# Performance work log

Hardware: AMD Instinct MI355X
Metric: run time of the kernel (lower is better)

Reference implementation:

```python
import jax, jax.numpy as jnp
import numpy as np

DIM = 64   # voxel grid resolution per axis
C = 64     # channels (C_in == num_outputs, required by residual add)
N = 200000 # number of points
EPS = 1e-3 # keras BatchNormalization default epsilon

def _bn(x, g, b, m, v):
    # inference-mode batch norm
    return (x - m) * jax.lax.rsqrt(v + EPS) * g + b

def _conv3d_relu(x, k, b):
    # x: [1,X,Y,Z,Cin], k: [3,3,3,Cin,Cout] (DHWIO), 'same' padding, relu activation
    y = jax.lax.conv_general_dilated(x, k, (1, 1, 1), 'SAME',
        dimension_numbers=('NDHWC', 'DHWIO', 'NDHWC'))
    return jax.nn.relu(y + b)

def _trilinear(grid, pts):
    # grid: [X,Y,Z,C], pts: [N,3] in voxel coordinates
    dmax = jnp.asarray(grid.shape[:3], pts.dtype) - 1.0
    p = jnp.clip(pts, 0.0, dmax)
    f = jnp.floor(p)
    t = p - f  # [N,3] fractional part
    i0 = f.astype(jnp.int32)
    i1 = jnp.minimum(i0 + 1, jnp.asarray(grid.shape[:3], jnp.int32) - 1)
    out = jnp.zeros((pts.shape[0], grid.shape[-1]), grid.dtype)
    for dx in (0, 1):
        for dy in (0, 1):
            for dz in (0, 1):
                ix = i1[:, 0] if dx else i0[:, 0]
                iy = i1[:, 1] if dy else i0[:, 1]
                iz = i1[:, 2] if dz else i0[:, 2]
                w = ((t[:, 0] if dx else 1.0 - t[:, 0])
                     * (t[:, 1] if dy else 1.0 - t[:, 1])
                     * (t[:, 2] if dz else 1.0 - t[:, 2]))
                out = out + w[:, None] * grid[ix, iy, iz]
    return out

def setup_inputs():
    key = jax.random.key(0)
    ks = jax.random.split(key, 10)
    inputs = jax.random.normal(ks[0], (N, C), jnp.float32)
    # pt_coords already scaled into voxel space (VOXEL_SIZE_INV folded in)
    pt_coords = jax.random.uniform(ks[1], (N, 3), jnp.float32) * (DIM - 1)
    voxel_indexes = jax.random.randint(ks[2], (N, 3), 0, DIM)
    pts_per_voxel_inv = jax.random.uniform(ks[3], (1, DIM, DIM, DIM, 1), jnp.float32)
    s = 1.0 / np.sqrt(C)
    w_mlp = jax.random.normal(ks[4], (C, C), jnp.float32) * s
    b_mlp = jnp.zeros((C,), jnp.float32)
    sk = 1.0 / np.sqrt(27 * C)
    k1 = jax.random.normal(ks[5], (3, 3, 3, C, C), jnp.float32) * sk
    cb1 = jnp.zeros((C,), jnp.float32)
    k2 = jax.random.normal(ks[6], (3, 3, 3, C, C), jnp.float32) * sk
    cb2 = jnp.zeros((C,), jnp.float32)
    def bn_params(k):
        a, b_, c = jax.random.split(k, 3)
        g = 1.0 + 0.1 * jax.random.normal(a, (C,), jnp.float32)
        be = 0.1 * jax.random.normal(b_, (C,), jnp.float32)
        m = 0.1 * jax.random.normal(c, (C,), jnp.float32)
        v = jnp.ones((C,), jnp.float32)
        return g, be, m, v
    g0, be0, m0, v0 = bn_params(ks[7])
    g1, be1, m1, v1 = bn_params(ks[8])
    g2, be2, m2, v2 = bn_params(ks[9])
    return dict(inputs=inputs, pt_coords=pt_coords, voxel_indexes=voxel_indexes,
                pts_per_voxel_inv=pts_per_voxel_inv, w_mlp=w_mlp, b_mlp=b_mlp,
                g0=g0, be0=be0, m0=m0, v0=v0, k1=k1, cb1=cb1, g1=g1, be1=be1,
                m1=m1, v1=v1, k2=k2, cb2=cb2, g2=g2, be2=be2, m2=m2, v2=v2)

def reference(inputs, pt_coords, voxel_indexes, pts_per_voxel_inv, w_mlp, b_mlp,
              g0, be0, m0, v0, k1, cb1, g1, be1, m1, v1, k2, cb2, g2, be2, m2, v2):
    # point branch: Dense(relu) + BN
    mlp_out = _bn(jax.nn.relu(inputs @ w_mlp + b_mlp), g0, be0, m0, v0)
    # voxelize: scatter_nd adds duplicate-index contributions
    voxels = jnp.zeros((DIM, DIM, DIM, C), inputs.dtype).at[
        voxel_indexes[:, 0], voxel_indexes[:, 1], voxel_indexes[:, 2]].add(inputs)
    voxels = voxels[None] * pts_per_voxel_inv  # per-voxel mean normalization
    # voxel branch: two Conv3D(relu)+BN
    h = _bn(_conv3d_relu(voxels, k1, cb1), g1, be1, m1, v1)
    h = _bn(_conv3d_relu(h, k2, cb2), g2, be2, m2, v2)
    # devoxelize: trilinear gather back to points (coords already in voxel space)
    vox_out = _trilinear(h[0], pt_coords)
    return mlp_out + vox_out
```

## Files before the change

### kernel.cpp

```cpp
#include <hip/hip_runtime.h>
#include <hip/hip_bf16.h>

#define DIMV 64
#define CH 64
#define EPSB 1e-3f

using bf16x8 = __attribute__((ext_vector_type(8))) short;
using f32x16 = __attribute__((ext_vector_type(16))) float;

__device__ __forceinline__ unsigned short f2bf(float f) {
    union { float f; unsigned u; } x; x.f = f;
    unsigned r = x.u + 0x7fff + ((x.u >> 16) & 1);
    return (unsigned short)(r >> 16);
}
__device__ __forceinline__ float bf2f(unsigned short u) {
    union { unsigned u; float f; } x; x.u = ((unsigned)u) << 16;
    return x.f;
}

__global__ __launch_bounds__(256) void mlp_mfma(
    const float* __restrict__ x, const unsigned short* __restrict__ wfrag,
    const float* __restrict__ b, const float* __restrict__ g,
    const float* __restrict__ be, const float* __restrict__ m,
    const float* __restrict__ v, float* __restrict__ out, int npts) {
    const int wid = blockIdx.x * 4 + (threadIdx.x >> 6);
    if (wid * 32 >= npts) return;
    const int lane = threadIdx.x & 63;
    const int col = lane & 31;
    const int kg = lane >> 5;
    const int p0 = wid * 32;

    bf16x8 a[4];
    const float* xr = x + (size_t)(p0 + col) * CH + kg * 8;
#pragma unroll
    for (int kk = 0; kk < 4; ++kk) {
        const float* p = xr + kk * 16;
        bf16x8 t;
#pragma unroll
        for (int j = 0; j < 8; ++j) t[j] = (short)f2bf(p[j]);
        a[kk] = t;
    }

    f32x16 acc[2];
#pragma unroll
    for (int nt = 0; nt < 2; ++nt)
#pragma unroll
        for (int r = 0; r < 16; ++r) acc[nt][r] = 0.f;

#pragma unroll
    for (int kk = 0; kk < 4; ++kk) {
        bf16x8 b0 = *(const bf16x8*)(wfrag + (kk * 2 + 0) * 512 + lane * 8);
        bf16x8 b1 = *(const bf16x8*)(wfrag + (kk * 2 + 1) * 512 + lane * 8);
        acc[0] = __builtin_amdgcn_mfma_f32_32x32x16_bf16(a[kk], b0, acc[0], 0, 0, 0);
        acc[1] = __builtin_amdgcn_mfma_f32_32x32x16_bf16(a[kk], b1, acc[1], 0, 0, 0);
    }

#pragma unroll
    for (int nt = 0; nt < 2; ++nt) {
        int co = nt * 32 + col;
        float scale = g[co] * rsqrtf(v[co] + EPSB);
        float shift = be[co] - m[co] * scale;
        float bias = b[co];
#pragma unroll
        for (int r = 0; r < 16; ++r) {
            int row = (r & 3) + 8 * (r >> 2) + 4 * kg;
            float val = fmaxf(acc[nt][r] + bias, 0.f) * scale + shift;
            out[(size_t)(p0 + row) * CH + co] = val;
        }
    }
}

__global__ void scatter_kernel(const float* __restrict__ x, const int* __restrict__ idx,
                               float* __restrict__ grid, int n_total) {
    int tid = blockIdx.x * blockDim.x + threadIdx.x;
    if (tid >= n_total) return;
    int n = tid >> 6, c = tid & 63;
    int ix = idx[n * 3 + 0], iy = idx[n * 3 + 1], iz = idx[n * 3 + 2];
    atomicAdd(&grid[(size_t)(((ix * DIMV) + iy) * DIMV + iz) * CH + c], x[tid]);
}

__global__ void pack_kernel(const float* __restrict__ A, const float* __restrict__ inv,
                            unsigned short* __restrict__ G1) {
    int t = blockIdx.x * 256 + threadIdx.x;
    if (t >= (DIMV * DIMV * DIMV * CH) / 8) return;
    int v = t >> 3, c8 = (t & 7) * 8;
    const float* src = A + (size_t)v * CH + c8;
    float s = inv[v];
    __align__(16) unsigned short tmp[8];
#pragma unroll
    for (int j = 0; j < 8; ++j) tmp[j] = f2bf(src[j] * s);
    *(int4*)(G1 + (size_t)t * 8) = *(const int4*)tmp;
}

__global__ void wprep_kernel(const float* __restrict__ K, unsigned short* __restrict__ wbuf) {
    int t = blockIdx.x * 256 + threadIdx.x;
    if (t >= 27 * 4 * 2 * 64 * 8) return;
    int j = t & 7;
    int l = (t >> 3) & 63;
    int nt = (t >> 9) & 1;
    int kkl = (t >> 10) & 3;
    int d = t >> 12;
    int ci = kkl * 16 + (l >> 5) * 8 + j;
    int co = nt * 32 + (l & 31);
    wbuf[t] = f2bf(K[((size_t)d * 64 + ci) * 64 + co]);
}

__global__ void wprep_mlp(const float* __restrict__ W, unsigned short* __restrict__ wm) {
    int t = blockIdx.x * 256 + threadIdx.x;
    if (t >= 4 * 2 * 64 * 8) return;
    int j = t & 7;
    int l = (t >> 3) & 63;
    int nt = (t >> 9) & 1;
    int kkl = (t >> 10) & 3;
    int ci = kkl * 16 + (l >> 5) * 8 + j;
    int co = nt * 32 + (l & 31);
    wm[t] = f2bf(W[(size_t)ci * 64 + co]);
}

template <typename OutT>
__global__ __launch_bounds__(256) void conv_mfma(
    const unsigned short* __restrict__ G, const unsigned short* __restrict__ wbuf,
    const float* __restrict__ cb, const float* __restrict__ g,
    const float* __restrict__ be, const float* __restrict__ m,
    const float* __restrict__ v, OutT* __restrict__ out) {
    __shared__ __align__(16) unsigned short slab[288 * 128];
    const int tid = threadIdx.x;
    const int lane = tid & 63;
    const int w = tid >> 6;
    const int wx = w >> 1, wy = w & 1;
    const int lz = lane & 31;
    const int kg = lane >> 5;
    const int BX = blockIdx.x, BY = blockIdx.y, BZ = blockIdx.z;
    const int x0 = 2 * BX - 1, y0 = 2 * BY - 1;
    const int zbase = 32 * BZ - 2;

#pragma unroll
    for (int it = 0; it < 18; ++it) {
        int idx = it * 256 + tid;
        int s = idx & 15;
        int r = idx >> 4;
        int zp = r % 18;
        int ryx = r / 18;
        int xx = x0 + (ryx >> 2);
        int yy = y0 + (ryx & 3);
        int cp = s ^ (zp & 15);
        int c = cp >> 1, p = cp & 1;
        int zz = zbase + 2 * zp + p;
        int4 val = make_int4(0, 0, 0, 0);
        if ((unsigned)xx < DIMV && (unsigned)yy < DIMV && (unsigned)zz < DIMV)
            val = *(const int4*)(G + (size_t)(((xx * DIMV) + yy) * DIMV + zz) * CH + c * 8);
        *(int4*)(slab + (size_t)idx * 8) = val;
    }
    __syncthreads();

    f32x16 acc[2];
#pragma unroll
    for (int nt = 0; nt < 2; ++nt)
#pragma unroll
        for (int r = 0; r < 16; ++r) acc[nt][r] = 0.f;

    bf16x8 bfr0[8], bfr1[8];
#pragma unroll
    for (int q = 0; q < 8; ++q)
        bfr0[q] = *(const bf16x8*)(wbuf + q * 512 + lane * 8);

#pragma unroll
    for (int d = 0; d < 27; ++d) {
        if (d < 26) {
            const unsigned short* wn = wbuf + (size_t)(d + 1) * 4096;
            if (d & 1) {
#pragma unroll
                for (int q = 0; q < 8; ++q) bfr0[q] = *(const bf16x8*)(wn + q * 512 + lane * 8);
            } else {
#pragma unroll
                for (int q = 0; q < 8; ++q) bfr1[q] = *(const bf16x8*)(wn + q * 512 + lane * 8);
            }
        }
        const int dx = d / 9, dy = (d / 3) % 3, dz = d % 3;
        const int zval = lz + dz + 1;
        const int zp = zval >> 1, p = zval & 1;
        const int r0 = ((wx + dx) * 4 + (wy + dy)) * 18 + zp;
#pragma unroll
        for (int kkl = 0; kkl < 4; ++kkl) {
            const int c = kkl * 2 + kg;
            const int slot = (c * 2 + p) ^ (zp & 15);
            bf16x8 a = *(const bf16x8*)(slab + r0 * 128 + slot * 8);
            bf16x8 b0 = (d & 1) ? bfr1[kkl * 2 + 0] : bfr0[kkl * 2 + 0];
            bf16x8 b1 = (d & 1) ? bfr1[kkl * 2 + 1] : bfr0[kkl * 2 + 1];
            acc[0] = __builtin_amdgcn_mfma_f32_32x32x16_bf16(a, b0, acc[0], 0, 0, 0);
            acc[1] = __builtin_amdgcn_mfma_f32_32x32x16_bf16(a, b1, acc[1], 0, 0, 0);
        }
    }

    const int x_out = 2 * BX + wx;
    const int y_out = 2 * BY + wy;
#pragma unroll
    for (int nt = 0; nt < 2; ++nt) {
        int co = nt * 32 + lz;
        float scale = g[co] * rsqrtf(v[co] + EPSB);
        float shift = be[co] - m[co] * scale;
        float bias = cb[co];
        size_t base = (size_t)((x_out * DIMV) + y_out) * DIMV * CH + co;
#pragma unroll
        for (int r = 0; r < 16; ++r) {
            int zrow = (r & 3) + 8 * (r >> 2) + 4 * kg;
            int z = BZ * 32 + zrow;
            float val = fmaxf(acc[nt][r] + bias, 0.f) * scale + shift;
            out[base + (size_t)z * CH] = f2bf(val);
        }
    }
}

__global__ void gather_kernel(const unsigned short* __restrict__ grid,
                              const float* __restrict__ pts,
                              float* __restrict__ out, int n_total) {
    int tid = blockIdx.x * blockDim.x + threadIdx.x;
    if (tid >= n_total) return;
    int n = tid >> 6, c = tid & 63;
    float px = fminf(fmaxf(pts[n * 3 + 0], 0.f), (float)(DIMV - 1));
    float py = fminf(fmaxf(pts[n * 3 + 1], 0.f), (float)(DIMV - 1));
    float pz = fminf(fmaxf(pts[n * 3 + 2], 0.f), (float)(DIMV - 1));
    float fx = floorf(px), fy = floorf(py), fz = floorf(pz);
    float tx = px - fx, ty = py - fy, tz = pz - fz;
    int x0 = (int)fx, y0 = (int)fy, z0 = (int)fz;
    int x1 = min(x0 + 1, DIMV - 1), y1 = min(y0 + 1, DIMV - 1), z1 = min(z0 + 1, DIMV - 1);
    float wx0 = 1.f - tx, wy0 = 1.f - ty, wz0 = 1.f - tz;

    float acc = 0.f;
    acc = fmaf(wx0 * wy0 * wz0, bf2f(grid[(size_t)(((x0 * DIMV) + y0) * DIMV + z0) * CH + c]), acc);
    acc = fmaf(wx0 * wy0 * tz,  bf2f(grid[(size_t)(((x0 * DIMV) + y0) * DIMV + z1) * CH + c]), acc);
    acc = fmaf(wx0 * ty * wz0,  bf2f(grid[(size_t)(((x0 * DIMV) + y1) * DIMV + z0) * CH + c]), acc);
    acc = fmaf(wx0 * ty * tz,   bf2f(grid[(size_t)(((x0 * DIMV) + y1) * DIMV + z1) * CH + c]), acc);
    acc = fmaf(tx * wy0 * wz0,  bf2f(grid[(size_t)(((x1 * DIMV) + y0) * DIMV + z0) * CH + c]), acc);
    acc = fmaf(tx * wy0 * tz,   bf2f(grid[(size_t)(((x1 * DIMV) + y0) * DIMV + z1) * CH + c]), acc);
    acc = fmaf(tx * ty * wz0,   bf2f(grid[(size_t)(((x1 * DIMV) + y1) * DIMV + z0) * CH + c]), acc);
    acc = fmaf(tx * ty * tz,    bf2f(grid[(size_t)(((x1 * DIMV) + y1) * DIMV + z1) * CH + c]), acc);
    out[tid] += acc;
}

extern "C" void kernel_launch(void* const* d_in, const int* in_sizes, int n_in,
                              void* d_out, int out_size, void* d_ws, size_t ws_size,
                              hipStream_t stream) {
    const float* inputs = (const float*)d_in[0];
    const float* pt_coords = (const float*)d_in[1];
    const int* voxel_indexes = (const int*)d_in[2];
    const float* ppvi = (const float*)d_in[3];
    const float* w_mlp = (const float*)d_in[4];
    const float* b_mlp = (const float*)d_in[5];
    const float* g0 = (const float*)d_in[6];
    const float* be0 = (const float*)d_in[7];
    const float* m0 = (const float*)d_in[8];
    const float* v0 = (const float*)d_in[9];
    const float* k1 = (const float*)d_in[10];
    const float* cb1 = (const float*)d_in[11];
    const float* g1 = (const float*)d_in[12];
    const float* be1 = (const float*)d_in[13];
    const float* m1 = (const float*)d_in[14];
    const float* v1 = (const float*)d_in[15];
    const float* k2 = (const float*)d_in[16];
    const float* cb2 = (const float*)d_in[17];
    const float* g2 = (const float*)d_in[18];
    const float* be2 = (const float*)d_in[19];
    const float* m2 = (const float*)d_in[20];
    const float* v2 = (const float*)d_in[21];
    float* out = (float*)d_out;

    char* ws = (char*)d_ws;
    float* A = (float*)ws;
    unsigned short* G2 = (unsigned short*)ws;
    unsigned short* G3 = (unsigned short*)(ws + 33554432);
    unsigned short* G1 = (unsigned short*)(ws + 67108864);
    unsigned short* wbuf1 = (unsigned short*)(ws + 100663296);
    unsigned short* wbuf2 = (unsigned short*)(ws + 100884480);
    unsigned short* wmlp = (unsigned short*)(ws + 101105664);

    const int n_total = in_sizes[0];
    const int npts = n_total / CH;
    const int nblk = (n_total + 255) / 256;
    const size_t grid_elems = (size_t)DIMV * DIMV * DIMV * CH;

    hipMemsetAsync(A, 0, grid_elems * sizeof(float), stream);
    wprep_mlp<<<16, 256, 0, stream>>>(w_mlp, wmlp);
    wprep_kernel<<<432, 256, 0, stream>>>(k1, wbuf1);
    wprep_kernel<<<432, 256, 0, stream>>>(k2, wbuf2);
    mlp_mfma<<<(npts / 32 + 3) / 4, 256, 0, stream>>>(inputs, wmlp, b_mlp, g0, be0, m0, v0, out, npts);
    scatter_kernel<<<nblk, 256, 0, stream>>>(inputs, voxel_indexes, A, n_total);
    pack_kernel<<<(int)(grid_elems / 8 + 255) / 256, 256, 0, stream>>>(A, ppvi, G1);

    dim3 cgrid(32, 32, 2);
    conv_mfma<unsigned short><<<cgrid, 256, 0, stream>>>(G1, wbuf1, cb1, g1, be1, m1, v1, G2);
    conv_mfma<unsigned short><<<cgrid, 256, 0, stream>>>(G2, wbuf2, cb2, g2, be2, m2, v2, G3);

    gather_kernel<<<nblk, 256, 0, stream>>>(G3, pt_coords, out, n_total);
}
```

Baseline: 301.1 us.

## Enlarge conv tile to 4x4 columns and fuse MLP into trilinear gather

The conv kernel now uses 512-thread blocks covering a 4x4 xy tile with a 6x6x34 halo slab. Each wave computes two y-columns, so every weight fragment feeds twice as many MFMAs and the halo overhead per output shrinks. The point MLP is fused into the gather kernel: MLP results are staged in LDS and added to the trilinear interpolation, which removes one full write and read-modify-write of the output. The trade-off is higher LDS use (about 153KB per conv block) and more accumulator registers, which could lower occupancy.

```diff
diff --git a/kernel.cpp b/kernel.cpp
--- a/kernel.cpp
+++ b/kernel.cpp
@@ -16,58 +16,6 @@
 __device__ __forceinline__ float bf2f(unsigned short u) {
     union { unsigned u; float f; } x; x.u = ((unsigned)u) << 16;
     return x.f;
-}
-
-__global__ __launch_bounds__(256) void mlp_mfma(
-    const float* __restrict__ x, const unsigned short* __restrict__ wfrag,
-    const float* __restrict__ b, const float* __restrict__ g,
-    const float* __restrict__ be, const float* __restrict__ m,
-    const float* __restrict__ v, float* __restrict__ out, int npts) {
-    const int wid = blockIdx.x * 4 + (threadIdx.x >> 6);
-    if (wid * 32 >= npts) return;
-    const int lane = threadIdx.x & 63;
-    const int col = lane & 31;
-    const int kg = lane >> 5;
-    const int p0 = wid * 32;
-
-    bf16x8 a[4];
-    const float* xr = x + (size_t)(p0 + col) * CH + kg * 8;
-#pragma unroll
-    for (int kk = 0; kk < 4; ++kk) {
-        const float* p = xr + kk * 16;
-        bf16x8 t;
-#pragma unroll
-        for (int j = 0; j < 8; ++j) t[j] = (short)f2bf(p[j]);
-        a[kk] = t;
-    }
-
-    f32x16 acc[2];
-#pragma unroll
-    for (int nt = 0; nt < 2; ++nt)
-#pragma unroll
-        for (int r = 0; r < 16; ++r) acc[nt][r] = 0.f;
-
-#pragma unroll
-    for (int kk = 0; kk < 4; ++kk) {
-        bf16x8 b0 = *(const bf16x8*)(wfrag + (kk * 2 + 0) * 512 + lane * 8);
-        bf16x8 b1 = *(const bf16x8*)(wfrag + (kk * 2 + 1) * 512 + lane * 8);
-        acc[0] = __builtin_amdgcn_mfma_f32_32x32x16_bf16(a[kk], b0, acc[0], 0, 0, 0);
-        acc[1] = __builtin_amdgcn_mfma_f32_32x32x16_bf16(a[kk], b1, acc[1], 0, 0, 0);
-    }
-
-#pragma unroll
-    for (int nt = 0; nt < 2; ++nt) {
-        int co = nt * 32 + col;
-        float scale = g[co] * rsqrtf(v[co] + EPSB);
-        float shift = be[co] - m[co] * scale;
-        float bias = b[co];
-#pragma unroll
-        for (int r = 0; r < 16; ++r) {
-            int row = (r & 3) + 8 * (r >> 2) + 4 * kg;
-            float val = fmaxf(acc[nt][r] + bias, 0.f) * scale + shift;
-            out[(size_t)(p0 + row) * CH + co] = val;
-        }
-    }
 }
 
 __global__ void scatter_kernel(const float* __restrict__ x, const int* __restrict__ idx,
@@ -117,47 +65,50 @@
     wm[t] = f2bf(W[(size_t)ci * 64 + co]);
 }
 
-template <typename OutT>
-__global__ __launch_bounds__(256) void conv_mfma(
+__global__ __launch_bounds__(512) void conv_mfma(
     const unsigned short* __restrict__ G, const unsigned short* __restrict__ wbuf,
     const float* __restrict__ cb, const float* __restrict__ g,
     const float* __restrict__ be, const float* __restrict__ m,
-    const float* __restrict__ v, OutT* __restrict__ out) {
-    __shared__ __align__(16) unsigned short slab[288 * 128];
+    const float* __restrict__ v, unsigned short* __restrict__ out) {
+    __shared__ __align__(16) unsigned short slab[612 * 128];
     const int tid = threadIdx.x;
     const int lane = tid & 63;
     const int w = tid >> 6;
-    const int wx = w >> 1, wy = w & 1;
+    const int cx = w >> 1;
+    const int cy0 = 2 * (w & 1);
     const int lz = lane & 31;
     const int kg = lane >> 5;
     const int BX = blockIdx.x, BY = blockIdx.y, BZ = blockIdx.z;
-    const int x0 = 2 * BX - 1, y0 = 2 * BY - 1;
-    const int zbase = 32 * BZ - 2;
-
-#pragma unroll
-    for (int it = 0; it < 18; ++it) {
-        int idx = it * 256 + tid;
-        int s = idx & 15;
-        int r = idx >> 4;
-        int zp = r % 18;
-        int ryx = r / 18;
-        int xx = x0 + (ryx >> 2);
-        int yy = y0 + (ryx & 3);
-        int cp = s ^ (zp & 15);
-        int c = cp >> 1, p = cp & 1;
-        int zz = zbase + 2 * zp + p;
-        int4 val = make_int4(0, 0, 0, 0);
-        if ((unsigned)xx < DIMV && (unsigned)yy < DIMV && (unsigned)zz < DIMV)
-            val = *(const int4*)(G + (size_t)(((xx * DIMV) + yy) * DIMV + zz) * CH + c * 8);
-        *(int4*)(slab + (size_t)idx * 8) = val;
+    const int x0 = 4 * BX - 1, y0 = 4 * BY - 1;
+    const int zbase = 32 * BZ - 1;
+
+    for (int it = 0; it < 20; ++it) {
+        int idx = it * 512 + tid;
+        if (idx < 9792) {
+            int s = idx & 15;
+            int r = idx >> 4;
+            int zp = r % 17;
+            int ryx = r / 17;
+            int xx = x0 + ryx / 6;
+            int yy = y0 + ryx % 6;
+            int cp = s ^ (zp & 15);
+            int c = cp >> 1, p = cp & 1;
+            int zz = zbase + 2 * zp + p;
+            int4 val = make_int4(0, 0, 0, 0);
+            if ((unsigned)xx < DIMV && (unsigned)yy < DIMV && (unsigned)zz < DIMV)
+                val = *(const int4*)(G + (size_t)(((xx * DIMV) + yy) * DIMV + zz) * CH + c * 8);
+            *(int4*)(slab + (size_t)idx * 8) = val;
+        }
     }
     __syncthreads();
 
-    f32x16 acc[2];
-#pragma unroll
-    for (int nt = 0; nt < 2; ++nt)
-#pragma unroll
-        for (int r = 0; r < 16; ++r) acc[nt][r] = 0.f;
+    f32x16 acc[2][2];
+#pragma unroll
+    for (int ct = 0; ct < 2; ++ct)
+#pragma unroll
+        for (int nt = 0; nt < 2; ++nt)
+#pragma unroll
+            for (int r = 0; r < 16; ++r) acc[ct][nt][r] = 0.f;
 
     bf16x8 bfr0[8], bfr1[8];
 #pragma unroll
@@ -177,65 +128,125 @@
             }
         }
         const int dx = d / 9, dy = (d / 3) % 3, dz = d % 3;
-        const int zval = lz + dz + 1;
+        const int zval = lz + dz;
         const int zp = zval >> 1, p = zval & 1;
-        const int r0 = ((wx + dx) * 4 + (wy + dy)) * 18 + zp;
+        const int rbase = ((cx + dx) * 6 + (cy0 + dy)) * 17 + zp;
 #pragma unroll
         for (int kkl = 0; kkl < 4; ++kkl) {
             const int c = kkl * 2 + kg;
             const int slot = (c * 2 + p) ^ (zp & 15);
-            bf16x8 a = *(const bf16x8*)(slab + r0 * 128 + slot * 8);
+            bf16x8 a0 = *(const bf16x8*)(slab + rbase * 128 + slot * 8);
+            bf16x8 a1 = *(const bf16x8*)(slab + (rbase + 17) * 128 + slot * 8);
             bf16x8 b0 = (d & 1) ? bfr1[kkl * 2 + 0] : bfr0[kkl * 2 + 0];
             bf16x8 b1 = (d & 1) ? bfr1[kkl * 2 + 1] : bfr0[kkl * 2 + 1];
-            acc[0] = __builtin_amdgcn_mfma_f32_32x32x16_bf16(a, b0, acc[0], 0, 0, 0);
-            acc[1] = __builtin_amdgcn_mfma_f32_32x32x16_bf16(a, b1, acc[1], 0, 0, 0);
-        }
-    }
-
-    const int x_out = 2 * BX + wx;
-    const int y_out = 2 * BY + wy;
-#pragma unroll
-    for (int nt = 0; nt < 2; ++nt) {
-        int co = nt * 32 + lz;
-        float scale = g[co] * rsqrtf(v[co] + EPSB);
-        float shift = be[co] - m[co] * scale;
-        float bias = cb[co];
-        size_t base = (size_t)((x_out * DIMV) + y_out) * DIMV * CH + co;
-#pragma unroll
-        for (int r = 0; r < 16; ++r) {
-            int zrow = (r & 3) + 8 * (r >> 2) + 4 * kg;
-            int z = BZ * 32 + zrow;
-            float val = fmaxf(acc[nt][r] + bias, 0.f) * scale + shift;
-            out[base + (size_t)z * CH] = f2bf(val);
-        }
-    }
-}
-
-__global__ void gather_kernel(const unsigned short* __restrict__ grid,
-                              const float* __restrict__ pts,
-                              float* __restrict__ out, int n_total) {
-    int tid = blockIdx.x * blockDim.x + threadIdx.x;
-    if (tid >= n_total) return;
-    int n = tid >> 6, c = tid & 63;
-    float px = fminf(fmaxf(pts[n * 3 + 0], 0.f), (float)(DIMV - 1));
-    float py = fminf(fmaxf(pts[n * 3 + 1], 0.f), (float)(DIMV - 1));
-    float pz = fminf(fmaxf(pts[n * 3 + 2], 0.f), (float)(DIMV - 1));
-    float fx = floorf(px), fy = floorf(py), fz = floorf(pz);
-    float tx = px - fx, ty = py - fy, tz = pz - fz;
-    int x0 = (int)fx, y0 = (int)fy, z0 = (int)fz;
-    int x1 = min(x0 + 1, DIMV - 1), y1 = min(y0 + 1, DIMV - 1), z1 = min(z0 + 1, DIMV - 1);
-    float wx0 = 1.f - tx, wy0 = 1.f - ty, wz0 = 1.f - tz;
-
-    float acc = 0.f;
-    acc = fmaf(wx0 * wy0 * wz0, bf2f(grid[(size_t)(((x0 * DIMV) + y0) * DIMV + z0) * CH + c]), acc);
-    acc = fmaf(wx0 * wy0 * tz,  bf2f(grid[(size_t)(((x0 * DIMV) + y0) * DIMV + z1) * CH + c]), acc);
-    acc = fmaf(wx0 * ty * wz0,  bf2f(grid[(size_t)(((x0 * DIMV) + y1) * DIMV + z0) * CH + c]), acc);
-    acc = fmaf(wx0 * ty * tz,   bf2f(grid[(size_t)(((x0 * DIMV) + y1) * DIMV + z1) * CH + c]), acc);
-    acc = fmaf(tx * wy0 * wz0,  bf2f(grid[(size_t)(((x1 * DIMV) + y0) * DIMV + z0) * CH + c]), acc);
-    acc = fmaf(tx * wy0 * tz,   bf2f(grid[(size_t)(((x1 * DIMV) + y0) * DIMV + z1) * CH + c]), acc);
-    acc = fmaf(tx * ty * wz0,   bf2f(grid[(size_t)(((x1 * DIMV) + y1) * DIMV + z0) * CH + c]), acc);
-    acc = fmaf(tx * ty * tz,    bf2f(grid[(size_t)(((x1 * DIMV) + y1) * DIMV + z1) * CH + c]), acc);
-    out[tid] += acc;
+            acc[0][0] = __builtin_amdgcn_mfma_f32_32x32x16_bf16(a0, b0, acc[0][0], 0, 0, 0);
+            acc[1][0] = __builtin_amdgcn_mfma_f32_32x32x16_bf16(a1, b0, acc[1][0], 0, 0, 0);
+            acc[0][1] = __builtin_amdgcn_mfma_f32_32x32x16_bf16(a0, b1, acc[0][1], 0, 0, 0);
+            acc[1][1] = __builtin_amdgcn_mfma_f32_32x32x16_bf16(a1, b1, acc[1][1], 0, 0, 0);
+        }
+    }
+
+    const int x_out = 4 * BX + cx;
+#pragma unroll
+    for (int ct = 0; ct < 2; ++ct) {
+        int y_out = 4 * BY + cy0 + ct;
+#pragma unroll
+        for (int nt = 0; nt < 2; ++nt) {
+            int co = nt * 32 + lz;
+            float scale = g[co] * rsqrtf(v[co] + EPSB);
+            float shift = be[co] - m[co] * scale;
+            float bias = cb[co];
+            size_t base = (size_t)((x_out * DIMV) + y_out) * DIMV * CH + co;
+#pragma unroll
+            for (int r = 0; r < 16; ++r) {
+                int zrow = (r & 3) + 8 * (r >> 2) + 4 * kg;
+                int z = BZ * 32 + zrow;
+                float val = fmaxf(acc[ct][nt][r] + bias, 0.f) * scale + shift;
+                out[base + (size_t)z * CH] = f2bf(val);
+            }
+        }
+    }
+}
+
+__global__ __launch_bounds__(256) void mlp_gather(
+    const float* __restrict__ x, const unsigned short* __restrict__ wfrag,
+    const float* __restrict__ b, const float* __restrict__ g,
+    const float* __restrict__ be, const float* __restrict__ m,
+    const float* __restrict__ v, const unsigned short* __restrict__ grid,
+    const float* __restrict__ pts, float* __restrict__ out, int npts) {
+    __shared__ float lds[128 * 64];
+    const int w = threadIdx.x >> 6;
+    const int lane = threadIdx.x & 63;
+    const int col = lane & 31;
+    const int kg = lane >> 5;
+    const int p0 = (blockIdx.x * 4 + w) * 32;
+
+    if (p0 < npts) {
+        bf16x8 a[4];
+        const float* xr = x + (size_t)(p0 + col) * CH + kg * 8;
+#pragma unroll
+        for (int kk = 0; kk < 4; ++kk) {
+            const float* p = xr + kk * 16;
+            bf16x8 t;
+#pragma unroll
+            for (int j = 0; j < 8; ++j) t[j] = (short)f2bf(p[j]);
+            a[kk] = t;
+        }
+        f32x16 acc[2];
+#pragma unroll
+        for (int nt = 0; nt < 2; ++nt)
+#pragma unroll
+            for (int r = 0; r < 16; ++r) acc[nt][r] = 0.f;
+#pragma unroll
+        for (int kk = 0; kk < 4; ++kk) {
+            bf16x8 b0 = *(const bf16x8*)(wfrag + (kk * 2 + 0) * 512 + lane * 8);
+            bf16x8 b1 = *(const bf16x8*)(wfrag + (kk * 2 + 1) * 512 + lane * 8);
+            acc[0] = __builtin_amdgcn_mfma_f32_32x32x16_bf16(a[kk], b0, acc[0], 0, 0, 0);
+            acc[1] = __builtin_amdgcn_mfma_f32_32x32x16_bf16(a[kk], b1, acc[1], 0, 0, 0);
+        }
+#pragma unroll
+        for (int nt = 0; nt < 2; ++nt) {
+            int co = nt * 32 + col;
+            float scale = g[co] * rsqrtf(v[co] + EPSB);
+            float shift = be[co] - m[co] * scale;
+            float bias = b[co];
+#pragma unroll
+            for (int r = 0; r < 16; ++r) {
+                int row = (r & 3) + 8 * (r >> 2) + 4 * kg;
+                float val = fmaxf(acc[nt][r] + bias, 0.f) * scale + shift;
+                lds[(w * 32 + row) * 64 + co] = val;
+            }
+        }
+    }
+    __syncthreads();
+
+    const int pblk = blockIdx.x * 128;
+#pragma unroll 4
+    for (int i = 0; i < 32; ++i) {
+        int idx = i * 256 + threadIdx.x;
+        int pl = idx >> 6;
+        int c = idx & 63;
+        int pt = pblk + pl;
+        if (pt >= npts) break;
+        float px = fminf(fmaxf(pts[pt * 3 + 0], 0.f), (float)(DIMV - 1));
+        float py = fminf(fmaxf(pts[pt * 3 + 1], 0.f), (float)(DIMV - 1));
+        float pz = fminf(fmaxf(pts[pt * 3 + 2], 0.f), (float)(DIMV - 1));
+        float fx = floorf(px), fy = floorf(py), fz = floorf(pz);
+        float tx = px - fx, ty = py - fy, tz = pz - fz;
+        int x0 = (int)fx, y0 = (int)fy, z0 = (int)fz;
+        int x1 = min(x0 + 1, DIMV - 1), y1 = min(y0 + 1, DIMV - 1), z1 = min(z0 + 1, DIMV - 1);
+        float wx0 = 1.f - tx, wy0 = 1.f - ty, wz0 = 1.f - tz;
+        float acc = lds[pl * 64 + c];
+        acc = fmaf(wx0 * wy0 * wz0, bf2f(grid[(size_t)(((x0 * DIMV) + y0) * DIMV + z0) * CH + c]), acc);
+        acc = fmaf(wx0 * wy0 * tz,  bf2f(grid[(size_t)(((x0 * DIMV) + y0) * DIMV + z1) * CH + c]), acc);
+        acc = fmaf(wx0 * ty * wz0,  bf2f(grid[(size_t)(((x0 * DIMV) + y1) * DIMV + z0) * CH + c]), acc);
+        acc = fmaf(wx0 * ty * tz,   bf2f(grid[(size_t)(((x0 * DIMV) + y1) * DIMV + z1) * CH + c]), acc);
+        acc = fmaf(tx * wy0 * wz0,  bf2f(grid[(size_t)(((x1 * DIMV) + y0) * DIMV + z0) * CH + c]), acc);
+        acc = fmaf(tx * wy0 * tz,   bf2f(grid[(size_t)(((x1 * DIMV) + y0) * DIMV + z1) * CH + c]), acc);
+        acc = fmaf(tx * ty * wz0,   bf2f(grid[(size_t)(((x1 * DIMV) + y1) * DIMV + z0) * CH + c]), acc);
+        acc = fmaf(tx * ty * tz,    bf2f(grid[(size_t)(((x1 * DIMV) + y1) * DIMV + z1) * CH + c]), acc);
+        out[(size_t)pt * CH + c] = acc;
+    }
 }
 
 extern "C" void kernel_launch(void* const* d_in, const int* in_sizes, int n_in,
@@ -283,13 +294,13 @@
     wprep_mlp<<<16, 256, 0, stream>>>(w_mlp, wmlp);
     wprep_kernel<<<432, 256, 0, stream>>>(k1, wbuf1);
     wprep_kernel<<<432, 256, 0, stream>>>(k2, wbuf2);
-    mlp_mfma<<<(npts / 32 + 3) / 4, 256, 0, stream>>>(inputs, wmlp, b_mlp, g0, be0, m0, v0, out, npts);
     scatter_kernel<<<nblk, 256, 0, stream>>>(inputs, voxel_indexes, A, n_total);
     pack_kernel<<<(int)(grid_elems / 8 + 255) / 256, 256, 0, stream>>>(A, ppvi, G1);
 
-    dim3 cgrid(32, 32, 2);
-    conv_mfma<unsigned short><<<cgrid, 256, 0, stream>>>(G1, wbuf1, cb1, g1, be1, m1, v1, G2);
-    conv_mfma<unsigned short><<<cgrid, 256, 0, stream>>>(G2, wbuf2, cb2, g2, be2, m2, v2, G3);
-
-    gather_kernel<<<nblk, 256, 0, stream>>>(G3, pt_coords, out, n_total);
-}
+    dim3 cgrid(16, 16, 2);
+    conv_mfma<<<cgrid, 512, 0, stream>>>(G1, wbuf1, cb1, g1, be1, m1, v1, G2);
+    conv_mfma<<<cgrid, 512, 0, stream>>>(G2, wbuf2, cb2, g2, be2, m2, v2, G3);
+
+    mlp_gather<<<(npts + 127) / 128, 256, 0, stream>>>(
+        inputs, wmlp, b_mlp, g0, be0, m0, v0, G3, pt_coords, out, npts);
+}
```

Result: faster. 283.4 us (-5.9%).
